# Kernel tuning notes

Hardware: AMD Instinct MI355X
Metric: run time of the kernel (lower is better)

## Reference

```python
import jax, jax.numpy as jnp
import numpy as np

NUM_HEADS = 16
HEAD_DIM = 64
KERNEL = 13  # odd
DIM = NUM_HEADS * HEAD_DIM
SCALE = HEAD_DIM ** -0.5


def setup_inputs() -> dict:
    key = jax.random.key(0)
    ks = jax.random.split(key, 6)
    B, L = 4, 4096
    return {
        "x": jax.random.normal(ks[0], (B, L, DIM), jnp.float32),
        "w_qkv": jax.random.normal(ks[1], (DIM, 3 * DIM), jnp.float32) * 0.02,
        "b_qkv": jax.random.normal(ks[2], (3 * DIM,), jnp.float32) * 0.02,
        "rpb": jax.random.normal(ks[3], (NUM_HEADS, 2 * KERNEL - 1), jnp.float32) * 0.02,
        "w_proj": jax.random.normal(ks[4], (DIM, DIM), jnp.float32) * 0.02,
        "b_proj": jax.random.normal(ks[5], (DIM,), jnp.float32) * 0.02,
    }


def _na1d(q, k, v, rpb, kernel_size):
    # q,k,v: [B,H,L,D]; rpb: [H, 2K-1]. dilation == 1.
    L = q.shape[2]
    K = kernel_size
    r = K // 2
    i = jnp.arange(L)
    # neighborhood start, clamped so each query sees exactly K keys (NATTEN semantics)
    ni = jnp.clip(i - r, 0, L - K)                    # [L]
    nbr = ni[:, None] + jnp.arange(K)                 # [L,K] key indices
    k_nb = k[:, :, nbr]                               # [B,H,L,K,D]
    attn = jnp.einsum("bhld,bhlkd->bhlk", q, k_nb)   # windowed QK
    # relative-position-bias start index: bias idx = (key_pos - i) + (K-1)
    pi = ni - i + (K - 1)                             # [L]
    bias = rpb[:, pi[:, None] + jnp.arange(K)]        # [H,L,K]
    attn = jax.nn.softmax(attn + bias[None], axis=-1)
    v_nb = v[:, :, nbr]                               # [B,H,L,K,D]
    return jnp.einsum("bhlk,bhlkd->bhld", attn, v_nb)


def reference(x, w_qkv, b_qkv, rpb, w_proj, b_proj):
    B, L, C = x.shape
    qkv = x @ w_qkv + b_qkv                           # [B,L,3C]
    qkv = qkv.reshape(B, L, 3, NUM_HEADS, HEAD_DIM).transpose(2, 0, 3, 1, 4)
    q, k, v = qkv[0] * SCALE, qkv[1], qkv[2]          # [B,H,L,D]
    out = _na1d(q, k, v, rpb, KERNEL)                 # [B,H,L,D]
    out = out.transpose(0, 2, 1, 3).reshape(B, L, C)
    return out @ w_proj + b_proj
```

## Files before the change

### kernel.cpp

```cpp
#include <hip/hip_runtime.h>

typedef __bf16 bf16x8_t __attribute__((ext_vector_type(8)));
typedef float  f32x4_t  __attribute__((ext_vector_type(4)));
typedef float  floatx4  __attribute__((ext_vector_type(4)));
typedef unsigned short ushortx4 __attribute__((ext_vector_type(4)));

__device__ __forceinline__ float bf2f(unsigned short u) {
    union { unsigned int i; float f; } c; c.i = ((unsigned int)u) << 16; return c.f;
}
__device__ __forceinline__ unsigned short f2bf(float f) {
    union { float f; unsigned int i; } c; c.f = f;
    unsigned int u = c.i;
    u += 0x7fffu + ((u >> 16) & 1u);
    return (unsigned short)(u >> 16);
}
__device__ __forceinline__ void unpack8(uint4 u, float* dst, float sc) {
    dst[0] = bf2f((unsigned short)(u.x & 0xffff)) * sc;
    dst[1] = bf2f((unsigned short)(u.x >> 16)) * sc;
    dst[2] = bf2f((unsigned short)(u.y & 0xffff)) * sc;
    dst[3] = bf2f((unsigned short)(u.y >> 16)) * sc;
    dst[4] = bf2f((unsigned short)(u.z & 0xffff)) * sc;
    dst[5] = bf2f((unsigned short)(u.z >> 16)) * sc;
    dst[6] = bf2f((unsigned short)(u.w & 0xffff)) * sc;
    dst[7] = bf2f((unsigned short)(u.w >> 16)) * sc;
}

__device__ __forceinline__ void load_lds16(const unsigned short* g, unsigned short* l) {
    __builtin_amdgcn_global_load_lds(
        (const __attribute__((address_space(1))) unsigned int*)g,
        (__attribute__((address_space(3))) unsigned int*)l, 16, 0, 0);
}

__global__ __launch_bounds__(256) void convert_f32_bf16(
    const float* __restrict__ x, unsigned short* __restrict__ xb)
{
    size_t i = ((size_t)blockIdx.x * 256 + threadIdx.x) * 8;
    floatx4 a = *reinterpret_cast<const floatx4*>(x + i);
    floatx4 b = *reinterpret_cast<const floatx4*>(x + i + 4);
    uint4 o;
    o.x = (unsigned int)f2bf(a.x) | ((unsigned int)f2bf(a.y) << 16);
    o.y = (unsigned int)f2bf(a.z) | ((unsigned int)f2bf(a.w) << 16);
    o.z = (unsigned int)f2bf(b.x) | ((unsigned int)f2bf(b.y) << 16);
    o.w = (unsigned int)f2bf(b.z) | ((unsigned int)f2bf(b.w) << 16);
    *reinterpret_cast<uint4*>(xb + i) = o;
}

__global__ __launch_bounds__(256) void transpose_f32_to_bf16(
    const float* __restrict__ W, unsigned short* __restrict__ Wt,
    int Kdim, int Ndim)
{
    __shared__ float tile[32][33];
    const int n0 = blockIdx.x * 32, k0 = blockIdx.y * 32;
    const int tx = threadIdx.x & 31, ty = threadIdx.x >> 5;
#pragma unroll
    for (int r = 0; r < 4; ++r) {
        int k = ty + r * 8;
        tile[k][tx] = W[(size_t)(k0 + k) * Ndim + n0 + tx];
    }
    __syncthreads();
#pragma unroll
    for (int r = 0; r < 4; ++r) {
        int n = ty + r * 8;
        Wt[(size_t)(n0 + n) * Kdim + k0 + tx] = f2bf(tile[tx][n]);
    }
}

#define BM 128
#define BN 128
#define BK 32

template<bool C_F32>
__global__ __launch_bounds__(256) void gemm_lds_kernel(
    const unsigned short* __restrict__ A, const unsigned short* __restrict__ Wt,
    const float* __restrict__ bias, void* __restrict__ Cp,
    int N, int K, int lda, int ldc)
{
    __shared__ __align__(16) unsigned short As[BM * BK];
    __shared__ __align__(16) unsigned short Bs[BN * BK];

    const int tid  = threadIdx.x;
    const int lane = tid & 63;
    const int wid  = tid >> 6;
    const int wm   = wid >> 1;
    const int wn   = wid & 1;
    const int quad = lane >> 4;
    const int lr   = lane & 15;

    const int m0 = blockIdx.y * BM;
    const int n0 = blockIdx.x * BN;

    const int s_row = tid >> 2;
    const int c_sw  = ((tid & 3) ^ ((tid >> 3) & 3)) * 8;
    const int xq    = (quad ^ ((lr >> 1) & 3)) * 8;
    unsigned short* ldsA = As + wid * 512;
    unsigned short* ldsB = Bs + wid * 512;

    f32x4_t acc[4][4];
#pragma unroll
    for (int i = 0; i < 4; ++i)
#pragma unroll
        for (int j = 0; j < 4; ++j)
            acc[i][j] = (f32x4_t){0.f, 0.f, 0.f, 0.f};

    for (int k0 = 0; k0 < K; k0 += BK) {
#pragma unroll
        for (int r = 0; r < 2; ++r) {
            load_lds16(A  + (size_t)(m0 + s_row + r * 64) * lda + k0 + c_sw, ldsA + r * 2048);
            load_lds16(Wt + (size_t)(n0 + s_row + r * 64) * K   + k0 + c_sw, ldsB + r * 2048);
        }
        __syncthreads();

        bf16x8_t av[4], bv[4];
#pragma unroll
        for (int i = 0; i < 4; ++i)
            av[i] = *reinterpret_cast<const bf16x8_t*>(&As[(wm * 64 + i * 16 + lr) * BK + xq]);
#pragma unroll
        for (int j = 0; j < 4; ++j)
            bv[j] = *reinterpret_cast<const bf16x8_t*>(&Bs[(wn * 64 + j * 16 + lr) * BK + xq]);

#pragma unroll
        for (int i = 0; i < 4; ++i)
#pragma unroll
            for (int j = 0; j < 4; ++j)
                acc[i][j] = __builtin_amdgcn_mfma_f32_16x16x32_bf16(av[i], bv[j], acc[i][j], 0, 0, 0);

        __syncthreads();
    }

#pragma unroll
    for (int j = 0; j < 4; ++j) {
        int col = n0 + wn * 64 + j * 16 + lr;
        float bj = bias[col];
#pragma unroll
        for (int i = 0; i < 4; ++i) {
            int rbase = m0 + wm * 64 + i * 16 + quad * 4;
#pragma unroll
            for (int r = 0; r < 4; ++r) {
                float v = acc[i][j][r] + bj;
                size_t idx = (size_t)(rbase + r) * ldc + col;
                if (C_F32) ((float*)Cp)[idx] = v;
                else       ((unsigned short*)Cp)[idx] = f2bf(v);
            }
        }
    }
}

#define LDT 40

template<bool A_F32, bool C_F32, bool BT>
__global__ __launch_bounds__(256) void gemm_bias_kernel(
    const void* __restrict__ Ap, const void* __restrict__ Wp,
    const float* __restrict__ bias, void* __restrict__ Cp,
    int N, int K, int lda, int ldc)
{
    __shared__ __align__(16) unsigned short As[BM * LDT];
    __shared__ __align__(16) unsigned short Bs[BN * LDT];

    const int tid  = threadIdx.x;
    const int lane = tid & 63;
    const int wid  = tid >> 6;
    const int wm   = wid >> 1;
    const int wn   = wid & 1;
    const int quad = lane >> 4;
    const int lr   = lane & 15;

    const int m0 = blockIdx.y * BM;
    const int n0 = blockIdx.x * BN;

    f32x4_t acc[4][4];
#pragma unroll
    for (int i = 0; i < 4; ++i)
#pragma unroll
        for (int j = 0; j < 4; ++j)
            acc[i][j] = (f32x4_t){0.f, 0.f, 0.f, 0.f};

    for (int k0 = 0; k0 < K; k0 += BK) {
        if (A_F32) {
            const float* A = (const float*)Ap;
#pragma unroll
            for (int it = 0; it < 4; ++it) {
                int q   = tid + it * 256;
                int row = q >> 3;
                int col = (q & 7) * 4;
                floatx4 f = *reinterpret_cast<const floatx4*>(A + (size_t)(m0 + row) * lda + k0 + col);
                ushortx4 s;
                s.x = f2bf(f.x); s.y = f2bf(f.y); s.z = f2bf(f.z); s.w = f2bf(f.w);
                *reinterpret_cast<ushortx4*>(&As[row * LDT + col]) = s;
            }
        } else {
            const unsigned short* A = (const unsigned short*)Ap;
            int a_row = tid >> 2;
            int a_col = (tid & 3) * 8;
#pragma unroll
            for (int r = 0; r < 2; ++r) {
                int row = a_row + r * 64;
                uint4 u = *reinterpret_cast<const uint4*>(A + (size_t)(m0 + row) * lda + k0 + a_col);
                *reinterpret_cast<uint4*>(&As[row * LDT + a_col]) = u;
            }
        }
        if (BT) {
            const unsigned short* Wt = (const unsigned short*)Wp;
            int b_row = tid >> 2;
            int b_col = (tid & 3) * 8;
#pragma unroll
            for (int r = 0; r < 2; ++r) {
                int n = b_row + r * 64;
                uint4 u = *reinterpret_cast<const uint4*>(Wt + (size_t)(n0 + n) * K + k0 + b_col);
                *reinterpret_cast<uint4*>(&Bs[n * LDT + b_col]) = u;
            }
        } else {
            const float* W = (const float*)Wp;
#pragma unroll
            for (int it = 0; it < 4; ++it) {
                int q  = tid + it * 256;
                int kk = q >> 5;
                int nn = (q & 31) * 4;
                floatx4 f = *reinterpret_cast<const floatx4*>(W + (size_t)(k0 + kk) * N + n0 + nn);
                Bs[(nn + 0) * LDT + kk] = f2bf(f.x);
                Bs[(nn + 1) * LDT + kk] = f2bf(f.y);
                Bs[(nn + 2) * LDT + kk] = f2bf(f.z);
                Bs[(nn + 3) * LDT + kk] = f2bf(f.w);
            }
        }
        __syncthreads();

        bf16x8_t av[4], bv[4];
#pragma unroll
        for (int i = 0; i < 4; ++i)
            av[i] = *reinterpret_cast<const bf16x8_t*>(&As[(wm * 64 + i * 16 + lr) * LDT + quad * 8]);
#pragma unroll
        for (int j = 0; j < 4; ++j)
            bv[j] = *reinterpret_cast<const bf16x8_t*>(&Bs[(wn * 64 + j * 16 + lr) * LDT + quad * 8]);

#pragma unroll
        for (int i = 0; i < 4; ++i)
#pragma unroll
            for (int j = 0; j < 4; ++j)
                acc[i][j] = __builtin_amdgcn_mfma_f32_16x16x32_bf16(av[i], bv[j], acc[i][j], 0, 0, 0);

        __syncthreads();
    }

#pragma unroll
    for (int j = 0; j < 4; ++j) {
        int col = n0 + wn * 64 + j * 16 + lr;
        float bj = bias[col];
#pragma unroll
        for (int i = 0; i < 4; ++i) {
            int rbase = m0 + wm * 64 + i * 16 + quad * 4;
#pragma unroll
            for (int r = 0; r < 4; ++r) {
                float v = acc[i][j][r] + bj;
                size_t idx = (size_t)(rbase + r) * ldc + col;
                if (C_F32) ((float*)Cp)[idx] = v;
                else       ((unsigned short*)Cp)[idx] = f2bf(v);
            }
        }
    }
}

#define NA_L 4096
#define NA_K 13
#define NA_H 16
#define NA_D 64
#define NA_SCALE 0.125f
#define TL  64
#define WIN 76
#define KD  68

__global__ __launch_bounds__(256) void na1d_tiled_kernel(
    unsigned short* qkv, const float* __restrict__ rpb)
{
    __shared__ __align__(16) float ks[WIN * KD];
    __shared__ __align__(16) float vs[WIN * KD];
    __shared__ __align__(16) float qs[TL * KD];
    __shared__ float wgt[TL][NA_K];

    const int bid = blockIdx.x;
    const int h  = bid & 15;
    const int lt = (bid >> 4) & 63;
    const int b  = bid >> 10;
    const int l0 = lt * TL;
    const int rs = l0 - 6;

    const int t = threadIdx.x;
    const size_t rowbase = (size_t)b * NA_L;

    {
        const int qr = t >> 2;
        const int qc = (t & 3) * 16;
        const unsigned short* qsrc = qkv + (rowbase + l0 + qr) * 3072 + h * 64 + qc;
        uint4 q0 = *reinterpret_cast<const uint4*>(qsrc);
        uint4 q1 = *reinterpret_cast<const uint4*>(qsrc + 8);

        const int r0 = t >> 3;
        const int cc = (t & 7) * 8;
        int g0 = rs + r0;      g0 = g0 < 0 ? 0 : (g0 > NA_L - 1 ? NA_L - 1 : g0);
        int g1 = rs + r0 + 32; g1 = g1 < 0 ? 0 : (g1 > NA_L - 1 ? NA_L - 1 : g1);
        const unsigned short* p0 = qkv + (rowbase + g0) * 3072 + 1024 + h * 64 + cc;
        const unsigned short* p1 = qkv + (rowbase + g1) * 3072 + 1024 + h * 64 + cc;
        uint4 k0 = *reinterpret_cast<const uint4*>(p0);
        uint4 v0 = *reinterpret_cast<const uint4*>(p0 + 1024);
        uint4 k1 = *reinterpret_cast<const uint4*>(p1);
        uint4 v1 = *reinterpret_cast<const uint4*>(p1 + 1024);
        uint4 k2, v2;
        if (t < 96) {
            int g2 = rs + r0 + 64; g2 = g2 < 0 ? 0 : (g2 > NA_L - 1 ? NA_L - 1 : g2);
            const unsigned short* p2 = qkv + (rowbase + g2) * 3072 + 1024 + h * 64 + cc;
            k2 = *reinterpret_cast<const uint4*>(p2);
            v2 = *reinterpret_cast<const uint4*>(p2 + 1024);
        }

        unpack8(q0, &qs[qr * KD + qc], NA_SCALE);
        unpack8(q1, &qs[qr * KD + qc + 8], NA_SCALE);
        unpack8(k0, &ks[r0 * KD + cc], 1.f);
        unpack8(v0, &vs[r0 * KD + cc], 1.f);
        unpack8(k1, &ks[(r0 + 32) * KD + cc], 1.f);
        unpack8(v1, &vs[(r0 + 32) * KD + cc], 1.f);
        if (t < 96) {
            unpack8(k2, &ks[(r0 + 64) * KD + cc], 1.f);
            unpack8(v2, &vs[(r0 + 64) * KD + cc], 1.f);
        }
    }
    __syncthreads();

    {
        const int l  = t & 63;
        const int jb = (t >> 6) * 4;
        int ig = l0 + l;
        int ni = ig - 6;
        if (ni < 0) ni = 0;
        if (ni > NA_L - NA_K) ni = NA_L - NA_K;
        int rid = ni - rs;
        int pi  = ni - ig + 12;
        const floatx4* qr = reinterpret_cast<const floatx4*>(&qs[l * KD]);
        const floatx4* k0 = reinterpret_cast<const floatx4*>(&ks[(rid + jb + 0) * KD]);
        const floatx4* k1 = reinterpret_cast<const floatx4*>(&ks[(rid + jb + 1) * KD]);
        const floatx4* k2 = reinterpret_cast<const floatx4*>(&ks[(rid + jb + 2) * KD]);
        const floatx4* k3 = reinterpret_cast<const floatx4*>(&ks[(rid + jb + 3) * KD]);
        floatx4 a0 = {0,0,0,0}, a1 = {0,0,0,0}, a2 = {0,0,0,0}, a3 = {0,0,0,0};
#pragma unroll
        for (int c = 0; c < 16; ++c) {
            floatx4 qv = qr[c];
            a0 += qv * k0[c];
            a1 += qv * k1[c];
            a2 += qv * k2[c];
            a3 += qv * k3[c];
        }
        float s0 = a0.x + a0.y + a0.z + a0.w;
        float s1 = a1.x + a1.y + a1.z + a1.w;
        float s2 = a2.x + a2.y + a2.z + a2.w;
        float s3 = a3.x + a3.y + a3.z + a3.w;
        const float* rp = rpb + h * 25 + pi;
        if (jb + 0 < NA_K) wgt[l][jb + 0] = s0 + rp[jb + 0];
        if (jb + 1 < NA_K) wgt[l][jb + 1] = s1 + rp[jb + 1];
        if (jb + 2 < NA_K) wgt[l][jb + 2] = s2 + rp[jb + 2];
        if (jb + 3 < NA_K) wgt[l][jb + 3] = s3 + rp[jb + 3];
    }
    __syncthreads();

    if (t < TL) {
        float m = -1e30f;
#pragma unroll
        for (int j = 0; j < NA_K; ++j) m = fmaxf(m, wgt[t][j]);
        float sum = 0.f;
#pragma unroll
        for (int j = 0; j < NA_K; ++j) {
            float e = expf(wgt[t][j] - m);
            wgt[t][j] = e;
            sum += e;
        }
        float inv = 1.f / sum;
#pragma unroll
        for (int j = 0; j < NA_K; ++j) wgt[t][j] *= inv;
    }
    __syncthreads();

    {
        const int l  = t & 63;
        const int d0 = (t >> 6) * 16;
        int ig = l0 + l;
        int ni = ig - 6;
        if (ni < 0) ni = 0;
        if (ni > NA_L - NA_K) ni = NA_L - NA_K;
        int rid = ni - rs;
        floatx4 o0 = {0,0,0,0}, o1 = {0,0,0,0}, o2 = {0,0,0,0}, o3 = {0,0,0,0};
#pragma unroll
        for (int j = 0; j < NA_K; ++j) {
            float w = wgt[l][j];
            const floatx4* vr = reinterpret_cast<const floatx4*>(&vs[(rid + j) * KD + d0]);
            o0 += w * vr[0];
            o1 += w * vr[1];
            o2 += w * vr[2];
            o3 += w * vr[3];
        }
        unsigned short* dst = qkv + (rowbase + ig) * 3072 + h * 64 + d0;
        uint4 p0, p1;
        p0.x = (unsigned int)f2bf(o0.x) | ((unsigned int)f2bf(o0.y) << 16);
        p0.y = (unsigned int)f2bf(o0.z) | ((unsigned int)f2bf(o0.w) << 16);
        p0.z = (unsigned int)f2bf(o1.x) | ((unsigned int)f2bf(o1.y) << 16);
        p0.w = (unsigned int)f2bf(o1.z) | ((unsigned int)f2bf(o1.w) << 16);
        p1.x = (unsigned int)f2bf(o2.x) | ((unsigned int)f2bf(o2.y) << 16);
        p1.y = (unsigned int)f2bf(o2.z) | ((unsigned int)f2bf(o2.w) << 16);
        p1.z = (unsigned int)f2bf(o3.x) | ((unsigned int)f2bf(o3.y) << 16);
        p1.w = (unsigned int)f2bf(o3.z) | ((unsigned int)f2bf(o3.w) << 16);
        *reinterpret_cast<uint4*>(dst)     = p0;
        *reinterpret_cast<uint4*>(dst + 8) = p1;
    }
}

extern "C" void kernel_launch(void* const* d_in, const int* in_sizes, int n_in,
                              void* d_out, int out_size, void* d_ws, size_t ws_size,
                              hipStream_t stream)
{
    const float* x      = (const float*)d_in[0];
    const float* w_qkv  = (const float*)d_in[1];
    const float* b_qkv  = (const float*)d_in[2];
    const float* rpb    = (const float*)d_in[3];
    const float* w_proj = (const float*)d_in[4];
    const float* b_proj = (const float*)d_in[5];
    float* out = (float*)d_out;

    const int M  = 4 * 4096;
    const int K  = 1024;
    const int N1 = 3072;
    const int N2 = 1024;

    unsigned short* qkv = (unsigned short*)d_ws;
    unsigned short* Wt1 = qkv + (size_t)M * N1;
    unsigned short* Wt2 = Wt1 + (size_t)N1 * K;
    unsigned short* xb  = Wt2 + (size_t)N2 * K;
    size_t need_mid  = ((size_t)M * N1 + (size_t)N1 * K + (size_t)N2 * K) * 2;
    size_t need_fast = need_mid + (size_t)M * K * 2;

    const int na_grid = 4 * (NA_L / TL) * NA_H;

    if (ws_size >= need_fast) {
        convert_f32_bf16<<<dim3(M * K / (256 * 8)), 256, 0, stream>>>(x, xb);
        transpose_f32_to_bf16<<<dim3(N1 / 32, K / 32), 256, 0, stream>>>(w_qkv, Wt1, K, N1);
        transpose_f32_to_bf16<<<dim3(N2 / 32, K / 32), 256, 0, stream>>>(w_proj, Wt2, K, N2);
        gemm_lds_kernel<false><<<dim3(N1 / BN, M / BM), 256, 0, stream>>>(
            xb, Wt1, b_qkv, qkv, N1, K, K, N1);
        na1d_tiled_kernel<<<dim3(na_grid), 256, 0, stream>>>(qkv, rpb);
        gemm_lds_kernel<true><<<dim3(N2 / BN, M / BM), 256, 0, stream>>>(
            qkv, Wt2, b_proj, out, N2, K, N1, N2);
    } else if (ws_size >= need_mid) {
        transpose_f32_to_bf16<<<dim3(N1 / 32, K / 32), 256, 0, stream>>>(w_qkv, Wt1, K, N1);
        transpose_f32_to_bf16<<<dim3(N2 / 32, K / 32), 256, 0, stream>>>(w_proj, Wt2, K, N2);
        gemm_bias_kernel<true, false, true><<<dim3(N1 / BN, M / BM), 256, 0, stream>>>(
            x, Wt1, b_qkv, qkv, N1, K, K, N1);
        na1d_tiled_kernel<<<dim3(na_grid), 256, 0, stream>>>(qkv, rpb);
        gemm_bias_kernel<false, true, true><<<dim3(N2 / BN, M / BM), 256, 0, stream>>>(
            qkv, Wt2, b_proj, out, N2, K, N1, N2);
    } else {
        gemm_bias_kernel<true, false, false><<<dim3(N1 / BN, M / BM), 256, 0, stream>>>(
            x, w_qkv, b_qkv, qkv, N1, K, K, N1);
        na1d_tiled_kernel<<<dim3(na_grid), 256, 0, stream>>>(qkv, rpb);
        gemm_bias_kernel<false, true, false><<<dim3(N2 / BN, M / BM), 256, 0, stream>>>(
            qkv, w_proj, b_proj, out, N2, K, N1, N2);
    }
}
```

Measured before the change: 410.5 us.

## Replace GEMM with 256x256-tile, 4-stage LDS-pipelined kernel with interleaved async loads

Replaces the 128x128 single-buffered LDS GEMM with a 512-thread, 256x256-tile kernel. It uses a 4-deep ring of LDS buffers and keeps three k-tiles of async global-to-LDS loads in flight. Loads are interleaved between MFMA groups, with explicit waitcnt, barriers, and setprio used to overlap memory with compute. The larger tile and deeper pipeline aim to hide load latency and raise data reuse, at the cost of 128KB of LDS per block, more registers, and fewer blocks for the N=1024 projection GEMM (256 blocks).

```diff
diff --git a/kernel.cpp b/kernel.cpp
--- a/kernel.cpp
+++ b/kernel.cpp
@@ -65,66 +65,106 @@
     }
 }
 
-#define BM 128
-#define BN 128
-#define BK 32
+#define TBM 256
+#define TBN 256
+#define TBK 32
 
 template<bool C_F32>
-__global__ __launch_bounds__(256) void gemm_lds_kernel(
+__global__ __launch_bounds__(512, 2) void gemm_pipe_kernel(
     const unsigned short* __restrict__ A, const unsigned short* __restrict__ Wt,
     const float* __restrict__ bias, void* __restrict__ Cp,
     int N, int K, int lda, int ldc)
 {
-    __shared__ __align__(16) unsigned short As[BM * BK];
-    __shared__ __align__(16) unsigned short Bs[BN * BK];
+    __shared__ __align__(16) unsigned short As[4][TBM * TBK];
+    __shared__ __align__(16) unsigned short Bs[4][TBN * TBK];
 
     const int tid  = threadIdx.x;
     const int lane = tid & 63;
     const int wid  = tid >> 6;
-    const int wm   = wid >> 1;
-    const int wn   = wid & 1;
+    const int wm   = wid >> 2;
+    const int wn   = wid & 3;
     const int quad = lane >> 4;
     const int lr   = lane & 15;
 
-    const int m0 = blockIdx.y * BM;
-    const int n0 = blockIdx.x * BN;
+    const int m0 = blockIdx.y * TBM;
+    const int n0 = blockIdx.x * TBN;
 
     const int s_row = tid >> 2;
     const int c_sw  = ((tid & 3) ^ ((tid >> 3) & 3)) * 8;
     const int xq    = (quad ^ ((lr >> 1) & 3)) * 8;
-    unsigned short* ldsA = As + wid * 512;
-    unsigned short* ldsB = Bs + wid * 512;
-
-    f32x4_t acc[4][4];
-#pragma unroll
-    for (int i = 0; i < 4; ++i)
+    const int NT    = K >> 5;
+
+    const unsigned short* Ag  = A  + (size_t)(m0 + s_row) * lda + c_sw;
+    const unsigned short* Ag2 = Ag + (size_t)128 * lda;
+    const unsigned short* Bg  = Wt + (size_t)(n0 + s_row) * K + c_sw;
+    const unsigned short* Bg2 = Bg + (size_t)128 * K;
+
+    f32x4_t acc[8][4];
+#pragma unroll
+    for (int i = 0; i < 8; ++i)
 #pragma unroll
         for (int j = 0; j < 4; ++j)
             acc[i][j] = (f32x4_t){0.f, 0.f, 0.f, 0.f};
 
-    for (int k0 = 0; k0 < K; k0 += BK) {
-#pragma unroll
-        for (int r = 0; r < 2; ++r) {
-            load_lds16(A  + (size_t)(m0 + s_row + r * 64) * lda + k0 + c_sw, ldsA + r * 2048);
-            load_lds16(Wt + (size_t)(n0 + s_row + r * 64) * K   + k0 + c_sw, ldsB + r * 2048);
-        }
-        __syncthreads();
-
-        bf16x8_t av[4], bv[4];
-#pragma unroll
-        for (int i = 0; i < 4; ++i)
-            av[i] = *reinterpret_cast<const bf16x8_t*>(&As[(wm * 64 + i * 16 + lr) * BK + xq]);
-#pragma unroll
-        for (int j = 0; j < 4; ++j)
-            bv[j] = *reinterpret_cast<const bf16x8_t*>(&Bs[(wn * 64 + j * 16 + lr) * BK + xq]);
-
-#pragma unroll
-        for (int i = 0; i < 4; ++i)
-#pragma unroll
-            for (int j = 0; j < 4; ++j)
-                acc[i][j] = __builtin_amdgcn_mfma_f32_16x16x32_bf16(av[i], bv[j], acc[i][j], 0, 0, 0);
-
-        __syncthreads();
+#pragma unroll
+    for (int tt = 0; tt < 3; ++tt) {
+        load_lds16(Ag  + tt * TBK, &As[tt][wid * 512]);
+        load_lds16(Ag2 + tt * TBK, &As[tt][4096 + wid * 512]);
+        load_lds16(Bg  + tt * TBK, &Bs[tt][wid * 512]);
+        load_lds16(Bg2 + tt * TBK, &Bs[tt][4096 + wid * 512]);
+    }
+    asm volatile("s_waitcnt vmcnt(8)" ::: "memory");
+    __builtin_amdgcn_s_barrier();
+    __builtin_amdgcn_sched_barrier(0);
+
+    for (int tt = 0; tt < NT; ++tt) {
+        const int b = tt & 3;
+        const unsigned short* pa = &As[b][0];
+        const unsigned short* pb = &Bs[b][0];
+        const bool st = (tt + 3) < NT;
+        const int  ts = tt + 3;
+        const int  sb = ts & 3;
+        bf16x8_t bv[4];
+
+#pragma unroll
+        for (int q = 0; q < 4; ++q) {
+            bf16x8_t a0 = *reinterpret_cast<const bf16x8_t*>(
+                pa + (wm * 128 + q * 32 + lr) * TBK + xq);
+            bf16x8_t a1 = *reinterpret_cast<const bf16x8_t*>(
+                pa + (wm * 128 + q * 32 + 16 + lr) * TBK + xq);
+            if (q == 0) {
+#pragma unroll
+                for (int j = 0; j < 4; ++j)
+                    bv[j] = *reinterpret_cast<const bf16x8_t*>(
+                        pb + (wn * 64 + j * 16 + lr) * TBK + xq);
+            }
+            if (st) {
+                if      (q == 0) load_lds16(Ag  + ts * TBK, &As[sb][wid * 512]);
+                else if (q == 1) load_lds16(Ag2 + ts * TBK, &As[sb][4096 + wid * 512]);
+                else if (q == 2) load_lds16(Bg  + ts * TBK, &Bs[sb][wid * 512]);
+                else             load_lds16(Bg2 + ts * TBK, &Bs[sb][4096 + wid * 512]);
+            }
+            __builtin_amdgcn_sched_barrier(0);
+            __builtin_amdgcn_s_barrier();
+            asm volatile("s_waitcnt lgkmcnt(0)" ::: "memory");
+            __builtin_amdgcn_sched_barrier(0);
+
+            __builtin_amdgcn_s_setprio(1);
+#pragma unroll
+            for (int j = 0; j < 4; ++j) {
+                acc[2 * q    ][j] = __builtin_amdgcn_mfma_f32_16x16x32_bf16(a0, bv[j], acc[2 * q    ][j], 0, 0, 0);
+                acc[2 * q + 1][j] = __builtin_amdgcn_mfma_f32_16x16x32_bf16(a1, bv[j], acc[2 * q + 1][j], 0, 0, 0);
+            }
+            __builtin_amdgcn_s_setprio(0);
+            __builtin_amdgcn_sched_barrier(0);
+
+            if (q == 3) {
+                if (tt < NT - 3)       asm volatile("s_waitcnt vmcnt(8)" ::: "memory");
+                else if (tt == NT - 3) asm volatile("s_waitcnt vmcnt(4)" ::: "memory");
+                else                   asm volatile("s_waitcnt vmcnt(0)" ::: "memory");
+            }
+            __builtin_amdgcn_s_barrier();
+        }
     }
 
 #pragma unroll
@@ -132,8 +172,8 @@
         int col = n0 + wn * 64 + j * 16 + lr;
         float bj = bias[col];
 #pragma unroll
-        for (int i = 0; i < 4; ++i) {
-            int rbase = m0 + wm * 64 + i * 16 + quad * 4;
+        for (int i = 0; i < 8; ++i) {
+            int rbase = m0 + wm * 128 + i * 16 + quad * 4;
 #pragma unroll
             for (int r = 0; r < 4; ++r) {
                 float v = acc[i][j][r] + bj;
@@ -145,6 +185,9 @@
     }
 }
 
+#define BM 128
+#define BN 128
+#define BK 32
 #define LDT 40
 
 template<bool A_F32, bool C_F32, bool BT>
@@ -439,10 +482,10 @@
         convert_f32_bf16<<<dim3(M * K / (256 * 8)), 256, 0, stream>>>(x, xb);
         transpose_f32_to_bf16<<<dim3(N1 / 32, K / 32), 256, 0, stream>>>(w_qkv, Wt1, K, N1);
         transpose_f32_to_bf16<<<dim3(N2 / 32, K / 32), 256, 0, stream>>>(w_proj, Wt2, K, N2);
-        gemm_lds_kernel<false><<<dim3(N1 / BN, M / BM), 256, 0, stream>>>(
+        gemm_pipe_kernel<false><<<dim3(N1 / TBN, M / TBM), 512, 0, stream>>>(
             xb, Wt1, b_qkv, qkv, N1, K, K, N1);
         na1d_tiled_kernel<<<dim3(na_grid), 256, 0, stream>>>(qkv, rpb);
-        gemm_lds_kernel<true><<<dim3(N2 / BN, M / BM), 256, 0, stream>>>(
+        gemm_pipe_kernel<true><<<dim3(N2 / TBN, M / TBM), 512, 0, stream>>>(
             qkv, Wt2, b_proj, out, N2, K, N1, N2);
     } else if (ws_size >= need_mid) {
         transpose_f32_to_bf16<<<dim3(N1 / 32, K / 32), 256, 0, stream>>>(w_qkv, Wt1, K, N1);
```

Result: slower. 422.3 us (+2.9%).
